# Kernel tuning notes

Hardware: AMD Instinct MI355X
Metric: run time of the kernel (lower is better)

Reference implementation:

```python
import jax, jax.numpy as jnp
import numpy as np

OBS_DIM = 768; H = 128; W = 128
OBJ_DIM = 128; REL_DIM = 64; N_SLOTS = 32; ACT_DIM = 16; HID = 256
EPS = 1e-8; DT = 0.1; N_ITERS = 3
REND_IN = OBJ_DIM * N_SLOTS + REL_DIM * N_SLOTS * N_SLOTS  # 69632


def _ln(x, g, b):
    m = x.mean(-1, keepdims=True)
    v = ((x - m) ** 2).mean(-1, keepdims=True)
    return (x - m) / jnp.sqrt(v + 1e-5) * g + b


def setup_inputs() -> dict:
    key = jax.random.key(0)
    ks = iter(jax.random.split(key, 48))

    def w(shape):
        fan = shape[-2] if len(shape) > 1 else shape[0]
        return jax.random.normal(next(ks), shape, jnp.float32) / np.sqrt(fan)

    d = {}
    d['obs'] = jax.random.normal(next(ks), (1, H, W, OBS_DIM), jnp.float32)
    d['action'] = jax.random.normal(next(ks), (1, ACT_DIM), jnp.float32)
    d['slot_noise'] = jax.random.normal(next(ks), (1, N_SLOTS, OBJ_DIM), jnp.float32)
    d['slots_mu'] = jax.random.normal(next(ks), (1, 1, OBJ_DIM), jnp.float32)
    d['slots_log_sigma'] = jax.random.normal(next(ks), (1, 1, OBJ_DIM), jnp.float32) * 0.1 - 1.0
    d['ln_in_g'] = jnp.ones((OBS_DIM,)); d['ln_in_b'] = jnp.zeros((OBS_DIM,))
    d['ln_s_g'] = jnp.ones((OBJ_DIM,)); d['ln_s_b'] = jnp.zeros((OBJ_DIM,))
    d['ln_m_g'] = jnp.ones((OBJ_DIM,)); d['ln_m_b'] = jnp.zeros((OBJ_DIM,))
    d['Wq'] = w((OBJ_DIM, OBJ_DIM)); d['Wk'] = w((OBS_DIM, OBJ_DIM)); d['Wv'] = w((OBS_DIM, OBJ_DIM))
    d['mlp_w1'] = w((OBJ_DIM, 2 * OBJ_DIM)); d['mlp_b1'] = jnp.zeros((2 * OBJ_DIM,))
    d['mlp_w2'] = w((2 * OBJ_DIM, OBJ_DIM)); d['mlp_b2'] = jnp.zeros((OBJ_DIM,))
    d['prop_w1'] = w((OBJ_DIM, HID)); d['prop_b1'] = jnp.zeros((HID,))
    d['prop_w2'] = w((HID, OBJ_DIM)); d['prop_b2'] = jnp.zeros((OBJ_DIM,))
    d['rel_w1'] = w((2 * OBJ_DIM, 2 * REL_DIM)); d['rel_b1'] = jnp.zeros((2 * REL_DIM,))
    d['rel_w2'] = w((2 * REL_DIM, REL_DIM)); d['rel_b2'] = jnp.zeros((REL_DIM,))
    d['dyn_w1'] = w((OBJ_DIM + ACT_DIM, HID)); d['dyn_b1'] = jnp.zeros((HID,))
    d['dyn_w2'] = w((HID, HID)); d['dyn_b2'] = jnp.zeros((HID,))
    d['dyn_w3'] = w((HID, OBJ_DIM)); d['dyn_b3'] = jnp.zeros((OBJ_DIM,))
    d['gravity'] = jnp.array([0.0, -9.8, 0.0], jnp.float32)
    d['rend_w1'] = w((REND_IN, 2 * OBS_DIM)); d['rend_b1'] = jnp.zeros((2 * OBS_DIM,))
    d['rend_w2'] = w((2 * OBS_DIM, OBS_DIM)); d['rend_b2'] = jnp.zeros((OBS_DIM,))
    return d


def reference(obs, action, slot_noise, slots_mu, slots_log_sigma,
              ln_in_g, ln_in_b, ln_s_g, ln_s_b, ln_m_g, ln_m_b,
              Wq, Wk, Wv, mlp_w1, mlp_b1, mlp_w2, mlp_b2,
              prop_w1, prop_b1, prop_w2, prop_b2,
              rel_w1, rel_b1, rel_w2, rel_b2,
              dyn_w1, dyn_b1, dyn_w2, dyn_b2, dyn_w3, dyn_b3,
              gravity, rend_w1, rend_b1, rend_w2, rend_b2):
    B = obs.shape[0]
    # --- slot attention over flattened feature map ---
    x = obs.reshape(B, -1, OBS_DIM)                 # [B, HW, C]
    x = _ln(x, ln_in_g, ln_in_b)
    k = x @ Wk                                      # [B, HW, D]
    v = x @ Wv                                      # [B, HW, D]
    slots = slots_mu + jnp.exp(slots_log_sigma) * slot_noise  # [B, S, D]
    scale = OBJ_DIM ** -0.5
    for _ in range(N_ITERS):
        prev = slots
        q = _ln(slots, ln_s_g, ln_s_b) @ Wq
        logits = jnp.einsum('bsd,bnd->bsn', q, k) * scale
        attn = jax.nn.softmax(logits, axis=1)       # softmax over slots (dim=1)
        attn = attn / (attn.sum(-1, keepdims=True) + EPS)
        slots = prev + jnp.einsum('bsn,bnd->bsd', attn, v)
        h = _ln(slots, ln_m_g, ln_m_b)
        slots = slots + (jax.nn.relu(h @ mlp_w1 + mlp_b1) @ mlp_w2 + mlp_b2)
    # --- object property decoding ---
    objects = jax.nn.relu(slots @ prop_w1 + prop_b1) @ prop_w2 + prop_b2  # [B, S, D]
    # --- pairwise relation encoding (O(S^2)) ---
    S = N_SLOTS
    oi = jnp.broadcast_to(objects[:, :, None, :], (B, S, S, OBJ_DIM))
    oj = jnp.broadcast_to(objects[:, None, :, :], (B, S, S, OBJ_DIM))
    pairs = jnp.concatenate([oi, oj], -1)            # [B, S, S, 2D]
    relations = jax.nn.relu(pairs @ rel_w1 + rel_b1) @ rel_w2 + rel_b2  # [B, S, S, REL]
    # --- scene graph takes batch element 0 (as in torch source) ---
    obj0 = objects[0:1]                              # [1, S, D]
    rel0 = relations[0]                              # [S, S, REL]
    # --- physics engine ---
    a = jnp.broadcast_to(action[:, None, :], (1, S, ACT_DIM))
    inp = jnp.concatenate([obj0, a], -1)
    h = jax.nn.relu(inp @ dyn_w1 + dyn_b1)
    h = jax.nn.relu(h @ dyn_w2 + dyn_b2)
    delta = h @ dyn_w3 + dyn_b3                      # [1, S, D]
    delta = delta.at[:, :, :3].add(gravity * DT)
    next_objects = obj0 + delta * DT                 # [1, S, D]
    # --- render next observation ---
    feat = jnp.concatenate([next_objects.reshape(1, -1), rel0.reshape(1, -1)], -1)
    next_obs = jax.nn.relu(feat @ rend_w1 + rend_b1) @ rend_w2 + rend_b2  # [1, OBS_DIM]
    return next_obs
```

## Files before the change

kernel.cpp:

```cpp
#include <hip/hip_runtime.h>
#include <hip/hip_bf16.h>
#include <math.h>

#define NPIX    16384
#define OBSD    768
#define OBJ     128
#define NS      32
#define HIDD    256
#define RELD    64
#define ACTD    16
#define QSCALE  0.08838834764831845f
#define LNEPS   1e-5f
#define ATEPS   1e-8f
#define DTC     0.1f

#define OFF_STATS 0
#define OFF_KV    (OFF_STATS + NPIX*2)
#define OFF_SLOTS (OFF_KV + NPIX*256)
#define OFF_Q     (OFF_SLOTS + 4096)
#define OFF_H     (OFF_Q + 4096)
#define OFF_APART (OFF_H + 4096)
#define OFF_OBJ   (OFF_APART + 256*4128)
#define OFF_FEAT  (OFF_OBJ + 4096)
#define OFF_P1    (OFF_FEAT + 69632)
#define OFF_HREND (OFF_P1 + 1024*1536)
#define OFF_P3    (OFF_HREND + 1536)

__global__ __launch_bounds__(256) void k_stats(const float* __restrict__ obs,
                                               float* __restrict__ stats)
{
    int lane = threadIdx.x & 63;
    int w    = threadIdx.x >> 6;
    int row  = blockIdx.x * 4 + w;
    const float* o = obs + (size_t)row * OBSD;
    float s = 0.f, s2 = 0.f;
    #pragma unroll
    for (int i = 0; i < 12; ++i) { float v = o[lane + 64*i]; s += v; s2 += v*v; }
    #pragma unroll
    for (int off = 32; off > 0; off >>= 1) {
        s  += __shfl_down(s,  off);
        s2 += __shfl_down(s2, off);
    }
    if (lane == 0) {
        float m   = s  * (1.f/OBSD);
        float var = s2 * (1.f/OBSD) - m*m;
        stats[row*2]   = m;
        stats[row*2+1] = rsqrtf(var + LNEPS);
    }
}

#define STA 129
__global__ __launch_bounds__(256) void k_kv(
    const float* __restrict__ obs, const float* __restrict__ stats,
    const float* __restrict__ g, const float* __restrict__ b,
    const float* __restrict__ Wk, const float* __restrict__ Wv,
    float* __restrict__ kv)
{
    __shared__ float As[32*STA];
    __shared__ float Bs[32*128];
    __shared__ float sm[128], sr[128];
    int t  = threadIdx.x;
    int m0 = blockIdx.x * 128;
    int nsel = blockIdx.y;
    const float* W = nsel ? Wv : Wk;
    int tx = t & 15, ty = t >> 4;
    float acc[8][8];
    #pragma unroll
    for (int i = 0; i < 8; ++i) {
        #pragma unroll
        for (int j = 0; j < 8; ++j) acc[i][j] = 0.f;
    }
    if (t < 128) { sm[t] = stats[(m0+t)*2]; sr[t] = stats[(m0+t)*2+1]; }

    for (int ks = 0; ks < 24; ++ks) {
        int k0 = ks * 32;
        __syncthreads();
        #pragma unroll
        for (int r = 0; r < 16; ++r) {
            int id = t + 256*r;
            int m  = id >> 5, kk = id & 31;
            float val = obs[(size_t)(m0+m)*OBSD + k0 + kk];
            val = (val - sm[m]) * sr[m] * g[k0+kk] + b[k0+kk];
            As[kk*STA + m] = val;
        }
        #pragma unroll
        for (int r = 0; r < 16; ++r) {
            int id = t + 256*r;
            int kk = id >> 7, jj = id & 127;
            Bs[kk*128 + jj] = W[(size_t)(k0+kk)*128 + jj];
        }
        __syncthreads();
        #pragma unroll
        for (int kk = 0; kk < 32; ++kk) {
            float a8[8], b8[8];
            #pragma unroll
            for (int i = 0; i < 8; ++i) a8[i] = As[kk*STA + ty*8 + i];
            float4 u0 = *(const float4*)&Bs[kk*128 + tx*8];
            float4 u1 = *(const float4*)&Bs[kk*128 + tx*8 + 4];
            b8[0]=u0.x; b8[1]=u0.y; b8[2]=u0.z; b8[3]=u0.w;
            b8[4]=u1.x; b8[5]=u1.y; b8[6]=u1.z; b8[7]=u1.w;
            #pragma unroll
            for (int i = 0; i < 8; ++i) {
                #pragma unroll
                for (int j = 0; j < 8; ++j)
                    acc[i][j] = fmaf(a8[i], b8[j], acc[i][j]);
            }
        }
    }
    #pragma unroll
    for (int i = 0; i < 8; ++i) {
        size_t row = (size_t)(m0 + ty*8 + i);
        float4 o0 = make_float4(acc[i][0], acc[i][1], acc[i][2], acc[i][3]);
        float4 o1 = make_float4(acc[i][4], acc[i][5], acc[i][6], acc[i][7]);
        *(float4*)&kv[row*256 + nsel*128 + tx*8]     = o0;
        *(float4*)&kv[row*256 + nsel*128 + tx*8 + 4] = o1;
    }
}

__global__ __launch_bounds__(256) void k_slots_init(
    const float* __restrict__ mu, const float* __restrict__ lsig,
    const float* __restrict__ noise, float* __restrict__ slots)
{
    int id = blockIdx.x * 256 + threadIdx.x;
    int d  = id & 127;
    slots[id] = mu[d] + expf(lsig[d]) * noise[id];
}

__global__ __launch_bounds__(128) void k_q(
    const float* __restrict__ slots, const float* __restrict__ Wq,
    const float* __restrict__ g, const float* __restrict__ b,
    float* __restrict__ qg)
{
    int s = blockIdx.x, t = threadIdx.x;
    float x = slots[s*128 + t];
    __shared__ float red[128];
    __shared__ float hh[128];
    red[t] = x; __syncthreads();
    for (int off = 64; off > 0; off >>= 1) { if (t < off) red[t] += red[t+off]; __syncthreads(); }
    float mean = red[0] * (1.f/128.f); __syncthreads();
    float dx = x - mean;
    red[t] = dx*dx; __syncthreads();
    for (int off = 64; off > 0; off >>= 1) { if (t < off) red[t] += red[t+off]; __syncthreads(); }
    float var = red[0] * (1.f/128.f);
    hh[t] = dx * rsqrtf(var + LNEPS) * g[t] + b[t];
    __syncthreads();
    float acc = 0.f;
    for (int d = 0; d < 128; ++d) acc = fmaf(hh[d], Wq[d*128 + t], acc);
    qg[s*128 + t] = acc;
}

#define STK 129
#define STQ 132
#define STT 36
__global__ __launch_bounds__(256) void k_attn(
    const float* __restrict__ kv, const float* __restrict__ qg,
    float* __restrict__ part)
{
    __shared__ float q_lds[NS*STQ];
    __shared__ float k_lds[64*STK];
    __shared__ float at[64*STT];
    int t   = threadIdx.x;
    int px0 = blockIdx.x * 64;
    #pragma unroll
    for (int r = 0; r < 16; ++r) {
        int id = t + 256*r;
        int s = id >> 7, d = id & 127;
        q_lds[s*STQ + d] = qg[id];
    }
    #pragma unroll
    for (int r = 0; r < 32; ++r) {
        int id = t + 256*r;
        int p = id >> 7, d = id & 127;
        k_lds[p*STK + d] = kv[(size_t)(px0+p)*256 + d];
    }
    __syncthreads();

    int wv = t >> 6, p = t & 63;
    float acc[8];
    #pragma unroll
    for (int u = 0; u < 8; ++u) acc[u] = 0.f;
    for (int dc = 0; dc < 4; ++dc) {
        float kr[32];
        #pragma unroll
        for (int d = 0; d < 32; ++d) kr[d] = k_lds[p*STK + dc*32 + d];
        #pragma unroll
        for (int u = 0; u < 8; ++u) {
            int s = u*4 + wv;
            const float* qp = &q_lds[s*STQ + dc*32];
            #pragma unroll
            for (int ii = 0; ii < 8; ++ii) {
                float4 q4 = *(const float4*)(qp + 4*ii);
                acc[u] = fmaf(q4.x, kr[4*ii+0], acc[u]);
                acc[u] = fmaf(q4.y, kr[4*ii+1], acc[u]);
                acc[u] = fmaf(q4.z, kr[4*ii+2], acc[u]);
                acc[u] = fmaf(q4.w, kr[4*ii+3], acc[u]);
            }
        }
    }
    #pragma unroll
    for (int u = 0; u < 8; ++u) at[p*STT + u*4 + wv] = acc[u] * QSCALE;
    __syncthreads();

    if (t < 64) {
        float mx = -1e30f;
        #pragma unroll
        for (int s = 0; s < NS; ++s) mx = fmaxf(mx, at[t*STT + s]);
        float smv = 0.f;
        #pragma unroll
        for (int s = 0; s < NS; ++s) { float e = expf(at[t*STT + s] - mx); at[t*STT + s] = e; smv += e; }
        float inv = 1.f / smv;
        #pragma unroll
        for (int s = 0; s < NS; ++s) at[t*STT + s] *= inv;
    }
    __syncthreads();

    int d = t & 127, sh = t >> 7;
    float u16[16];
    #pragma unroll
    for (int i = 0; i < 16; ++i) u16[i] = 0.f;
    const float* vbase = kv + (size_t)px0*256 + 128 + d;
    #pragma unroll 4
    for (int pp = 0; pp < 64; ++pp) {
        float vv = vbase[(size_t)pp*256];
        const float4* ap = (const float4*)&at[pp*STT + sh*16];
        #pragma unroll
        for (int gg = 0; gg < 4; ++gg) {
            float4 a4 = ap[gg];
            u16[4*gg+0] = fmaf(a4.x, vv, u16[4*gg+0]);
            u16[4*gg+1] = fmaf(a4.y, vv, u16[4*gg+1]);
            u16[4*gg+2] = fmaf(a4.z, vv, u16[4*gg+2]);
            u16[4*gg+3] = fmaf(a4.w, vv, u16[4*gg+3]);
        }
    }
    float* P = part + (size_t)blockIdx.x * 4128;
    #pragma unroll
    for (int g2 = 0; g2 < 16; ++g2) P[(sh*16 + g2)*128 + d] = u16[g2];
    if (t < 32) {
        float ss = 0.f;
        for (int pp = 0; pp < 64; ++pp) ss += at[pp*STT + t];
        P[4096 + t] = ss;
    }
}

__global__ __launch_bounds__(128) void k_update(
    const float* __restrict__ part, float* __restrict__ slots,
    float* __restrict__ hm, const float* __restrict__ g, const float* __restrict__ b)
{
    int s = blockIdx.x, t = threadIdx.x;
    float u = 0.f, ss = 0.f;
    for (int bb = 0; bb < 256; ++bb) {
        const float* P = part + (size_t)bb * 4128;
        u  += P[s*128 + t];
        ss += P[4096 + s];
    }
    float x = slots[s*128 + t] + u / (ss + ATEPS);
    __shared__ float red[128];
    red[t] = x; __syncthreads();
    for (int off = 64; off > 0; off >>= 1) { if (t < off) red[t] += red[t+off]; __syncthreads(); }
    float mean = red[0] * (1.f/128.f); __syncthreads();
    float dx = x - mean;
    red[t] = dx*dx; __syncthreads();
    for (int off = 64; off > 0; off >>= 1) { if (t < off) red[t] += red[t+off]; __syncthreads(); }
    float var = red[0] * (1.f/128.f);
    slots[s*128 + t] = x;
    hm[s*128 + t] = dx * rsqrtf(var + LNEPS) * g[t] + b[t];
}

__global__ __launch_bounds__(256) void k_mlp(
    const float* __restrict__ hm, const float* __restrict__ w1, const float* __restrict__ b1,
    const float* __restrict__ w2, const float* __restrict__ b2, float* __restrict__ slots)
{
    int s = blockIdx.x, t = threadIdx.x;
    __shared__ float h[128], hid[256];
    if (t < 128) h[t] = hm[s*128 + t];
    __syncthreads();
    float a = b1[t];
    for (int d = 0; d < 128; ++d) a = fmaf(h[d], w1[d*256 + t], a);
    hid[t] = fmaxf(a, 0.f);
    __syncthreads();
    if (t < 128) {
        float o = b2[t];
        for (int j = 0; j < 256; ++j) o = fmaf(hid[j], w2[j*128 + t], o);
        slots[s*128 + t] += o;
    }
}

__global__ __launch_bounds__(256) void k_prop(
    const float* __restrict__ slots, const float* __restrict__ w1, const float* __restrict__ b1,
    const float* __restrict__ w2, const float* __restrict__ b2, float* __restrict__ objects)
{
    int s = blockIdx.x, t = threadIdx.x;
    __shared__ float h[128], hid[256];
    if (t < 128) h[t] = slots[s*128 + t];
    __syncthreads();
    float a = b1[t];
    for (int d = 0; d < 128; ++d) a = fmaf(h[d], w1[d*256 + t], a);
    hid[t] = fmaxf(a, 0.f);
    __syncthreads();
    if (t < 128) {
        float o = b2[t];
        for (int j = 0; j < 256; ++j) o = fmaf(hid[j], w2[j*128 + t], o);
        objects[s*128 + t] = o;
    }
}

__global__ __launch_bounds__(128) void k_rel(
    const float* __restrict__ objects, const float* __restrict__ w1, const float* __restrict__ b1,
    const float* __restrict__ w2, const float* __restrict__ b2, float* __restrict__ rel_out)
{
    int pr = blockIdx.x; int i = pr >> 5, j = pr & 31; int t = threadIdx.x;
    __shared__ float pair[256], hid[128];
    pair[t]       = objects[i*128 + t];
    pair[128 + t] = objects[j*128 + t];
    __syncthreads();
    float a = b1[t];
    for (int c = 0; c < 256; ++c) a = fmaf(pair[c], w1[c*128 + t], a);
    hid[t] = fmaxf(a, 0.f);
    __syncthreads();
    if (t < 64) {
        float o = b2[t];
        for (int c = 0; c < 128; ++c) o = fmaf(hid[c], w2[c*64 + t], o);
        rel_out[(size_t)pr*64 + t] = o;
    }
}

__global__ __launch_bounds__(256) void k_dyn(
    const float* __restrict__ objects, const float* __restrict__ action,
    const float* __restrict__ w1, const float* __restrict__ b1,
    const float* __restrict__ w2, const float* __restrict__ b2,
    const float* __restrict__ w3, const float* __restrict__ b3,
    const float* __restrict__ gravity, float* __restrict__ feat)
{
    int s = blockIdx.x, t = threadIdx.x;
    __shared__ float inp[144], h1[256], h2[256];
    if (t < 128) inp[t] = objects[s*128 + t];
    else if (t < 144) inp[t] = action[t - 128];
    __syncthreads();
    float a = b1[t];
    for (int c = 0; c < 144; ++c) a = fmaf(inp[c], w1[c*256 + t], a);
    h1[t] = fmaxf(a, 0.f);
    __syncthreads();
    float a2 = b2[t];
    for (int c = 0; c < 256; ++c) a2 = fmaf(h1[c], w2[c*256 + t], a2);
    h2[t] = fmaxf(a2, 0.f);
    __syncthreads();
    if (t < 128) {
        float dlt = b3[t];
        for (int c = 0; c < 256; ++c) dlt = fmaf(h2[c], w3[c*128 + t], dlt);
        if (t < 3) dlt += gravity[t] * DTC;
        feat[s*128 + t] = objects[s*128 + t] + dlt * DTC;
    }
}

__global__ __launch_bounds__(384) void k_rend1(
    const float* __restrict__ feat, const float* __restrict__ w1, float* __restrict__ p1)
{
    int b = blockIdx.x, t = threadIdx.x;
    float4 acc = make_float4(0.f, 0.f, 0.f, 0.f);
    int i0 = b * 68;
    #pragma unroll 4
    for (int r = 0; r < 68; ++r) {
        int i = i0 + r;
        float f = feat[i];
        float4 w = *(const float4*)(w1 + (size_t)i * 1536 + 4*t);
        acc.x = fmaf(f, w.x, acc.x);
        acc.y = fmaf(f, w.y, acc.y);
        acc.z = fmaf(f, w.z, acc.z);
        acc.w = fmaf(f, w.w, acc.w);
    }
    *(float4*)(p1 + (size_t)b * 1536 + 4*t) = acc;
}

__global__ __launch_bounds__(256) void k_rend2(
    const float* __restrict__ p1, const float* __restrict__ b1, float* __restrict__ h)
{
    int j = blockIdx.x * 256 + threadIdx.x;
    float a0 = 0.f, a1 = 0.f, a2 = 0.f, a3 = 0.f;
    #pragma unroll 4
    for (int bb = 0; bb < 1024; bb += 4) {
        a0 += p1[(size_t)(bb+0)*1536 + j];
        a1 += p1[(size_t)(bb+1)*1536 + j];
        a2 += p1[(size_t)(bb+2)*1536 + j];
        a3 += p1[(size_t)(bb+3)*1536 + j];
    }
    h[j] = fmaxf((a0+a1) + (a2+a3) + b1[j], 0.f);
}

__global__ __launch_bounds__(256) void k_rend3(
    const float* __restrict__ h, const float* __restrict__ w2, float* __restrict__ p3)
{
    int bj = blockIdx.x, t = threadIdx.x;
    int j0 = bj * 32;
    float a0 = 0.f, a1 = 0.f, a2 = 0.f;
    #pragma unroll
    for (int j = 0; j < 32; ++j) {
        float hj = h[j0 + j];
        const float* w = w2 + (size_t)(j0 + j) * 768;
        a0 = fmaf(hj, w[t],       a0);
        a1 = fmaf(hj, w[t + 256], a1);
        a2 = fmaf(hj, w[t + 512], a2);
    }
    p3[(size_t)bj*768 + t]       = a0;
    p3[(size_t)bj*768 + t + 256] = a1;
    p3[(size_t)bj*768 + t + 512] = a2;
}

__global__ __launch_bounds__(256) void k_rend4(
    const float* __restrict__ p3, const float* __restrict__ b2, float* __restrict__ out)
{
    int m = blockIdx.x * 256 + threadIdx.x;
    float a = b2[m];
    #pragma unroll
    for (int bj = 0; bj < 48; ++bj) a += p3[(size_t)bj*768 + m];
    out[m] = a;
}

extern "C" void kernel_launch(void* const* d_in, const int* in_sizes, int n_in,
                              void* d_out, int out_size, void* d_ws, size_t ws_size,
                              hipStream_t stream) {
    (void)in_sizes; (void)n_in; (void)out_size; (void)ws_size;
    const float* obs      = (const float*)d_in[0];
    const float* action   = (const float*)d_in[1];
    const float* noise    = (const float*)d_in[2];
    const float* mu       = (const float*)d_in[3];
    const float* lsig     = (const float*)d_in[4];
    const float* ln_in_g  = (const float*)d_in[5];
    const float* ln_in_b  = (const float*)d_in[6];
    const float* ln_s_g   = (const float*)d_in[7];
    const float* ln_s_b   = (const float*)d_in[8];
    const float* ln_m_g   = (const float*)d_in[9];
    const float* ln_m_b   = (const float*)d_in[10];
    const float* Wq       = (const float*)d_in[11];
    const float* Wk       = (const float*)d_in[12];
    const float* Wv       = (const float*)d_in[13];
    const float* mlp_w1   = (const float*)d_in[14];
    const float* mlp_b1   = (const float*)d_in[15];
    const float* mlp_w2   = (const float*)d_in[16];
    const float* mlp_b2   = (const float*)d_in[17];
    const float* prop_w1  = (const float*)d_in[18];
    const float* prop_b1  = (const float*)d_in[19];
    const float* prop_w2  = (const float*)d_in[20];
    const float* prop_b2  = (const float*)d_in[21];
    const float* rel_w1   = (const float*)d_in[22];
    const float* rel_b1   = (const float*)d_in[23];
    const float* rel_w2   = (const float*)d_in[24];
    const float* rel_b2   = (const float*)d_in[25];
    const float* dyn_w1   = (const float*)d_in[26];
    const float* dyn_b1   = (const float*)d_in[27];
    const float* dyn_w2   = (const float*)d_in[28];
    const float* dyn_b2   = (const float*)d_in[29];
    const float* dyn_w3   = (const float*)d_in[30];
    const float* dyn_b3   = (const float*)d_in[31];
    const float* gravity  = (const float*)d_in[32];
    const float* rend_w1  = (const float*)d_in[33];
    const float* rend_b1  = (const float*)d_in[34];
    const float* rend_w2  = (const float*)d_in[35];
    const float* rend_b2  = (const float*)d_in[36];
    float* out = (float*)d_out;

    float* w      = (float*)d_ws;
    float* stats  = w + OFF_STATS;
    float* kv     = w + OFF_KV;
    float* slots  = w + OFF_SLOTS;
    float* qg     = w + OFF_Q;
    float* hm     = w + OFF_H;
    float* apart  = w + OFF_APART;
    float* objs   = w + OFF_OBJ;
    float* feat   = w + OFF_FEAT;
    float* relout = feat + 4096;
    float* p1     = w + OFF_P1;
    float* hrend  = w + OFF_HREND;
    float* p3     = w + OFF_P3;

    k_stats<<<4096, 256, 0, stream>>>(obs, stats);
    k_kv<<<dim3(128, 2), 256, 0, stream>>>(obs, stats, ln_in_g, ln_in_b, Wk, Wv, kv);
    k_slots_init<<<16, 256, 0, stream>>>(mu, lsig, noise, slots);

    for (int it = 0; it < 3; ++it) {
        k_q<<<32, 128, 0, stream>>>(slots, Wq, ln_s_g, ln_s_b, qg);
        k_attn<<<256, 256, 0, stream>>>(kv, qg, apart);
        k_update<<<32, 128, 0, stream>>>(apart, slots, hm, ln_m_g, ln_m_b);
        k_mlp<<<32, 256, 0, stream>>>(hm, mlp_w1, mlp_b1, mlp_w2, mlp_b2, slots);
    }

    k_prop<<<32, 256, 0, stream>>>(slots, prop_w1, prop_b1, prop_w2, prop_b2, objs);
    k_rel<<<1024, 128, 0, stream>>>(objs, rel_w1, rel_b1, rel_w2, rel_b2, relout);
    k_dyn<<<32, 256, 0, stream>>>(objs, action, dyn_w1, dyn_b1, dyn_w2, dyn_b2,
                                  dyn_w3, dyn_b3, gravity, feat);

    k_rend1<<<1024, 384, 0, stream>>>(feat, rend_w1, p1);
    k_rend2<<<6, 256, 0, stream>>>(p1, rend_b1, hrend);
    k_rend3<<<48, 256, 0, stream>>>(hrend, rend_w2, p3);
    k_rend4<<<3, 256, 0, stream>>>(p3, rend_b2, out);
}
```

Baseline: 1.105 ms.

## Double-buffer KV GEMM, fuse slot update/MLP/query and prop/dyn, split render reduction

The K/V projection GEMM now double-buffers its shared tiles with register prefetch and vectorized A reads, so global loads overlap compute and one barrier per k-step is dropped. The slot update, LayerNorm, MLP and next-iteration query projection are fused into one kernel, and the prop and dynamics MLPs are merged, which cuts several small launches. The render reduction over 1024 partials, previously done by only 6 blocks, is split into a two-stage reduction to expose more parallelism. Risks include higher register use in k_kv (launch bounds 256,1) and the extra syncs in the fused kernels.

```diff
diff --git a/kernel.cpp b/kernel.cpp
--- a/kernel.cpp
+++ b/kernel.cpp
@@ -25,6 +25,7 @@
 #define OFF_P1    (OFF_FEAT + 69632)
 #define OFF_HREND (OFF_P1 + 1024*1536)
 #define OFF_P3    (OFF_HREND + 1536)
+#define OFF_P2    (OFF_P3 + 48*768)
 
 __global__ __launch_bounds__(256) void k_stats(const float* __restrict__ obs,
                                                float* __restrict__ stats)
@@ -49,56 +50,71 @@
     }
 }
 
-#define STA 129
-__global__ __launch_bounds__(256) void k_kv(
+#define KVA 132
+__global__ __launch_bounds__(256, 1) void k_kv(
     const float* __restrict__ obs, const float* __restrict__ stats,
     const float* __restrict__ g, const float* __restrict__ b,
     const float* __restrict__ Wk, const float* __restrict__ Wv,
     float* __restrict__ kv)
 {
-    __shared__ float As[32*STA];
-    __shared__ float Bs[32*128];
-    __shared__ float sm[128], sr[128];
-    int t  = threadIdx.x;
-    int m0 = blockIdx.x * 128;
+    __shared__ float As[2][32*KVA];
+    __shared__ float Bs[2][32*128];
+    int t    = threadIdx.x;
+    int m0   = blockIdx.x * 128;
     int nsel = blockIdx.y;
     const float* W = nsel ? Wv : Wk;
     int tx = t & 15, ty = t >> 4;
+    int ka = t & 31, ma = t >> 5;
+    int jb = t & 127, kb = t >> 7;
+
     float acc[8][8];
     #pragma unroll
     for (int i = 0; i < 8; ++i) {
         #pragma unroll
         for (int j = 0; j < 8; ++j) acc[i][j] = 0.f;
     }
-    if (t < 128) { sm[t] = stats[(m0+t)*2]; sr[t] = stats[(m0+t)*2+1]; }
+
+    float smr[16], srr[16];
+    #pragma unroll
+    for (int r = 0; r < 16; ++r) {
+        smr[r] = stats[(size_t)(m0 + ma + 8*r)*2];
+        srr[r] = stats[(size_t)(m0 + ma + 8*r)*2 + 1];
+    }
+
+    float pa[16], pb[16], gv, cv;
+    #pragma unroll
+    for (int r = 0; r < 16; ++r) pa[r] = obs[(size_t)(m0 + ma + 8*r)*OBSD + ka];
+    #pragma unroll
+    for (int r = 0; r < 16; ++r) pb[r] = W[(size_t)(kb + 2*r)*128 + jb];
+    gv = g[ka]; cv = b[ka];
+    #pragma unroll
+    for (int r = 0; r < 16; ++r)
+        As[0][ka*KVA + ma + 8*r] = (pa[r] - smr[r]) * srr[r] * gv + cv;
+    #pragma unroll
+    for (int r = 0; r < 16; ++r)
+        Bs[0][(kb + 2*r)*128 + jb] = pb[r];
+    __syncthreads();
 
     for (int ks = 0; ks < 24; ++ks) {
-        int k0 = ks * 32;
-        __syncthreads();
-        #pragma unroll
-        for (int r = 0; r < 16; ++r) {
-            int id = t + 256*r;
-            int m  = id >> 5, kk = id & 31;
-            float val = obs[(size_t)(m0+m)*OBSD + k0 + kk];
-            val = (val - sm[m]) * sr[m] * g[k0+kk] + b[k0+kk];
-            As[kk*STA + m] = val;
+        int cur = ks & 1;
+        if (ks < 23) {
+            int k0 = (ks + 1) * 32;
+            #pragma unroll
+            for (int r = 0; r < 16; ++r)
+                pa[r] = obs[(size_t)(m0 + ma + 8*r)*OBSD + k0 + ka];
+            #pragma unroll
+            for (int r = 0; r < 16; ++r)
+                pb[r] = W[(size_t)(k0 + kb + 2*r)*128 + jb];
+            gv = g[k0 + ka]; cv = b[k0 + ka];
         }
         #pragma unroll
-        for (int r = 0; r < 16; ++r) {
-            int id = t + 256*r;
-            int kk = id >> 7, jj = id & 127;
-            Bs[kk*128 + jj] = W[(size_t)(k0+kk)*128 + jj];
-        }
-        __syncthreads();
-        #pragma unroll
         for (int kk = 0; kk < 32; ++kk) {
-            float a8[8], b8[8];
-            #pragma unroll
-            for (int i = 0; i < 8; ++i) a8[i] = As[kk*STA + ty*8 + i];
-            float4 u0 = *(const float4*)&Bs[kk*128 + tx*8];
-            float4 u1 = *(const float4*)&Bs[kk*128 + tx*8 + 4];
-            b8[0]=u0.x; b8[1]=u0.y; b8[2]=u0.z; b8[3]=u0.w;
-            b8[4]=u1.x; b8[5]=u1.y; b8[6]=u1.z; b8[7]=u1.w;
+            float4 a0 = *(const float4*)&As[cur][kk*KVA + ty*8];
+            float4 a1 = *(const float4*)&As[cur][kk*KVA + ty*8 + 4];
+            float4 u0 = *(const float4*)&Bs[cur][kk*128 + tx*8];
+            float4 u1 = *(const float4*)&Bs[cur][kk*128 + tx*8 + 4];
+            float a8[8] = {a0.x,a0.y,a0.z,a0.w,a1.x,a1.y,a1.z,a1.w};
+            float b8[8] = {u0.x,u0.y,u0.z,u0.w,u1.x,u1.y,u1.z,u1.w};
             #pragma unroll
             for (int i = 0; i < 8; ++i) {
                 #pragma unroll
@@ -106,7 +122,18 @@
                     acc[i][j] = fmaf(a8[i], b8[j], acc[i][j]);
             }
         }
-    }
+        if (ks < 23) {
+            int nb = cur ^ 1;
+            #pragma unroll
+            for (int r = 0; r < 16; ++r)
+                As[nb][ka*KVA + ma + 8*r] = (pa[r] - smr[r]) * srr[r] * gv + cv;
+            #pragma unroll
+            for (int r = 0; r < 16; ++r)
+                Bs[nb][(kb + 2*r)*128 + jb] = pb[r];
+        }
+        __syncthreads();
+    }
+
     #pragma unroll
     for (int i = 0; i < 8; ++i) {
         size_t row = (size_t)(m0 + ty*8 + i);
@@ -242,65 +269,126 @@
     }
 }
 
-__global__ __launch_bounds__(128) void k_update(
+__global__ __launch_bounds__(256) void k_umq(
     const float* __restrict__ part, float* __restrict__ slots,
-    float* __restrict__ hm, const float* __restrict__ g, const float* __restrict__ b)
+    const float* __restrict__ gm, const float* __restrict__ bm,
+    const float* __restrict__ w1, const float* __restrict__ b1,
+    const float* __restrict__ w2, const float* __restrict__ b2,
+    const float* __restrict__ gs, const float* __restrict__ bs,
+    const float* __restrict__ Wq, float* __restrict__ qg, int do_q)
 {
     int s = blockIdx.x, t = threadIdx.x;
+    int d = t & 127, half = t >> 7;
+    __shared__ float red[256];
+    __shared__ float ssred[2];
+    __shared__ float xs[128], hm[128], hid[256];
+
     float u = 0.f, ss = 0.f;
-    for (int bb = 0; bb < 256; ++bb) {
-        const float* P = part + (size_t)bb * 4128;
-        u  += P[s*128 + t];
+    const float* P0 = part + (size_t)(half * 128) * 4128;
+    for (int bb = 0; bb < 128; ++bb) {
+        const float* P = P0 + (size_t)bb * 4128;
+        u  += P[s*128 + d];
         ss += P[4096 + s];
     }
-    float x = slots[s*128 + t] + u / (ss + ATEPS);
-    __shared__ float red[128];
-    red[t] = x; __syncthreads();
-    for (int off = 64; off > 0; off >>= 1) { if (t < off) red[t] += red[t+off]; __syncthreads(); }
-    float mean = red[0] * (1.f/128.f); __syncthreads();
-    float dx = x - mean;
-    red[t] = dx*dx; __syncthreads();
-    for (int off = 64; off > 0; off >>= 1) { if (t < off) red[t] += red[t+off]; __syncthreads(); }
-    float var = red[0] * (1.f/128.f);
-    slots[s*128 + t] = x;
-    hm[s*128 + t] = dx * rsqrtf(var + LNEPS) * g[t] + b[t];
-}
-
-__global__ __launch_bounds__(256) void k_mlp(
-    const float* __restrict__ hm, const float* __restrict__ w1, const float* __restrict__ b1,
-    const float* __restrict__ w2, const float* __restrict__ b2, float* __restrict__ slots)
+    red[t] = u;
+    if (d == 0) ssred[half] = ss;
+    __syncthreads();
+    if (half == 0)
+        xs[d] = slots[s*128 + d] + (red[d] + red[d+128]) / (ssred[0] + ssred[1] + ATEPS);
+    __syncthreads();
+
+    red[t] = (half == 0) ? xs[d] : 0.f;
+    __syncthreads();
+    #pragma unroll
+    for (int off = 128; off > 0; off >>= 1) { if (t < off) red[t] += red[t+off]; __syncthreads(); }
+    float mean = red[0] * (1.f/128.f);
+    __syncthreads();
+    { float dx = (half == 0) ? (xs[d] - mean) : 0.f; red[t] = dx*dx; }
+    __syncthreads();
+    #pragma unroll
+    for (int off = 128; off > 0; off >>= 1) { if (t < off) red[t] += red[t+off]; __syncthreads(); }
+    float rstd = rsqrtf(red[0] * (1.f/128.f) + LNEPS);
+    __syncthreads();
+    if (half == 0) hm[d] = (xs[d] - mean) * rstd * gm[d] + bm[d];
+    __syncthreads();
+
+    float a = b1[t];
+    for (int c = 0; c < 128; ++c) a = fmaf(hm[c], w1[c*256 + t], a);
+    hid[t] = fmaxf(a, 0.f);
+    __syncthreads();
+    if (half == 0) {
+        float o = b2[d];
+        for (int j = 0; j < 256; ++j) o = fmaf(hid[j], w2[j*128 + d], o);
+        float xn = xs[d] + o;
+        slots[s*128 + d] = xn;
+        xs[d] = xn;
+    }
+    __syncthreads();
+
+    if (do_q) {
+        red[t] = (half == 0) ? xs[d] : 0.f;
+        __syncthreads();
+        #pragma unroll
+        for (int off = 128; off > 0; off >>= 1) { if (t < off) red[t] += red[t+off]; __syncthreads(); }
+        float m2 = red[0] * (1.f/128.f);
+        __syncthreads();
+        { float dx = (half == 0) ? (xs[d] - m2) : 0.f; red[t] = dx*dx; }
+        __syncthreads();
+        #pragma unroll
+        for (int off = 128; off > 0; off >>= 1) { if (t < off) red[t] += red[t+off]; __syncthreads(); }
+        float r2 = rsqrtf(red[0] * (1.f/128.f) + LNEPS);
+        __syncthreads();
+        if (half == 0) hm[d] = (xs[d] - m2) * r2 * gs[d] + bs[d];
+        __syncthreads();
+        float acc = 0.f;
+        for (int c = half*64; c < half*64 + 64; ++c) acc = fmaf(hm[c], Wq[c*128 + d], acc);
+        red[t] = acc;
+        __syncthreads();
+        if (half == 0) qg[s*128 + d] = red[d] + red[d+128];
+    }
+}
+
+__global__ __launch_bounds__(256) void k_propdyn(
+    const float* __restrict__ slots,
+    const float* __restrict__ pw1, const float* __restrict__ pb1,
+    const float* __restrict__ pw2, const float* __restrict__ pb2,
+    const float* __restrict__ action,
+    const float* __restrict__ dw1, const float* __restrict__ db1,
+    const float* __restrict__ dw2, const float* __restrict__ db2,
+    const float* __restrict__ dw3, const float* __restrict__ db3,
+    const float* __restrict__ gravity,
+    float* __restrict__ objects, float* __restrict__ feat)
 {
     int s = blockIdx.x, t = threadIdx.x;
-    __shared__ float h[128], hid[256];
-    if (t < 128) h[t] = hm[s*128 + t];
-    __syncthreads();
-    float a = b1[t];
-    for (int d = 0; d < 128; ++d) a = fmaf(h[d], w1[d*256 + t], a);
+    __shared__ float h[128], hid[256], inp[144], h2[256];
+    if (t < 128) h[t] = slots[s*128 + t];
+    __syncthreads();
+    float a = pb1[t];
+    for (int c = 0; c < 128; ++c) a = fmaf(h[c], pw1[c*256 + t], a);
     hid[t] = fmaxf(a, 0.f);
     __syncthreads();
     if (t < 128) {
-        float o = b2[t];
-        for (int j = 0; j < 256; ++j) o = fmaf(hid[j], w2[j*128 + t], o);
-        slots[s*128 + t] += o;
-    }
-}
-
-__global__ __launch_bounds__(256) void k_prop(
-    const float* __restrict__ slots, const float* __restrict__ w1, const float* __restrict__ b1,
-    const float* __restrict__ w2, const float* __restrict__ b2, float* __restrict__ objects)
-{
-    int s = blockIdx.x, t = threadIdx.x;
-    __shared__ float h[128], hid[256];
-    if (t < 128) h[t] = slots[s*128 + t];
-    __syncthreads();
-    float a = b1[t];
-    for (int d = 0; d < 128; ++d) a = fmaf(h[d], w1[d*256 + t], a);
-    hid[t] = fmaxf(a, 0.f);
+        float o = pb2[t];
+        for (int j = 0; j < 256; ++j) o = fmaf(hid[j], pw2[j*128 + t], o);
+        objects[s*128 + t] = o;
+        inp[t] = o;
+    } else if (t < 144) {
+        inp[t] = action[t - 128];
+    }
+    __syncthreads();
+    float a1 = db1[t];
+    for (int c = 0; c < 144; ++c) a1 = fmaf(inp[c], dw1[c*256 + t], a1);
+    hid[t] = fmaxf(a1, 0.f);
+    __syncthreads();
+    float a2 = db2[t];
+    for (int c = 0; c < 256; ++c) a2 = fmaf(hid[c], dw2[c*256 + t], a2);
+    h2[t] = fmaxf(a2, 0.f);
     __syncthreads();
     if (t < 128) {
-        float o = b2[t];
-        for (int j = 0; j < 256; ++j) o = fmaf(hid[j], w2[j*128 + t], o);
-        objects[s*128 + t] = o;
+        float dlt = db3[t];
+        for (int c = 0; c < 256; ++c) dlt = fmaf(h2[c], dw3[c*128 + t], dlt);
+        if (t < 3) dlt += gravity[t] * DTC;
+        feat[s*128 + t] = inp[t] + dlt * DTC;
     }
 }
 
@@ -321,34 +409,6 @@
         float o = b2[t];
         for (int c = 0; c < 128; ++c) o = fmaf(hid[c], w2[c*64 + t], o);
         rel_out[(size_t)pr*64 + t] = o;
-    }
-}
-
-__global__ __launch_bounds__(256) void k_dyn(
-    const float* __restrict__ objects, const float* __restrict__ action,
-    const float* __restrict__ w1, const float* __restrict__ b1,
-    const float* __restrict__ w2, const float* __restrict__ b2,
-    const float* __restrict__ w3, const float* __restrict__ b3,
-    const float* __restrict__ gravity, float* __restrict__ feat)
-{
-    int s = blockIdx.x, t = threadIdx.x;
-    __shared__ float inp[144], h1[256], h2[256];
-    if (t < 128) inp[t] = objects[s*128 + t];
-    else if (t < 144) inp[t] = action[t - 128];
-    __syncthreads();
-    float a = b1[t];
-    for (int c = 0; c < 144; ++c) a = fmaf(inp[c], w1[c*256 + t], a);
-    h1[t] = fmaxf(a, 0.f);
-    __syncthreads();
-    float a2 = b2[t];
-    for (int c = 0; c < 256; ++c) a2 = fmaf(h1[c], w2[c*256 + t], a2);
-    h2[t] = fmaxf(a2, 0.f);
-    __syncthreads();
-    if (t < 128) {
-        float dlt = b3[t];
-        for (int c = 0; c < 256; ++c) dlt = fmaf(h2[c], w3[c*128 + t], dlt);
-        if (t < 3) dlt += gravity[t] * DTC;
-        feat[s*128 + t] = objects[s*128 + t] + dlt * DTC;
     }
 }
 
@@ -371,19 +431,31 @@
     *(float4*)(p1 + (size_t)b * 1536 + 4*t) = acc;
 }
 
-__global__ __launch_bounds__(256) void k_rend2(
-    const float* __restrict__ p1, const float* __restrict__ b1, float* __restrict__ h)
-{
-    int j = blockIdx.x * 256 + threadIdx.x;
+__global__ __launch_bounds__(256) void k_rend2a(
+    const float* __restrict__ p1, float* __restrict__ p2)
+{
+    int j  = blockIdx.x * 256 + threadIdx.x;
+    int sl = blockIdx.y;
+    const float* P = p1 + (size_t)sl * 64 * 1536;
     float a0 = 0.f, a1 = 0.f, a2 = 0.f, a3 = 0.f;
     #pragma unroll 4
-    for (int bb = 0; bb < 1024; bb += 4) {
-        a0 += p1[(size_t)(bb+0)*1536 + j];
-        a1 += p1[(size_t)(bb+1)*1536 + j];
-        a2 += p1[(size_t)(bb+2)*1536 + j];
-        a3 += p1[(size_t)(bb+3)*1536 + j];
-    }
-    h[j] = fmaxf((a0+a1) + (a2+a3) + b1[j], 0.f);
+    for (int bb = 0; bb < 64; bb += 4) {
+        a0 += P[(size_t)(bb+0)*1536 + j];
+        a1 += P[(size_t)(bb+1)*1536 + j];
+        a2 += P[(size_t)(bb+2)*1536 + j];
+        a3 += P[(size_t)(bb+3)*1536 + j];
+    }
+    p2[sl*1536 + j] = (a0+a1) + (a2+a3);
+}
+
+__global__ __launch_bounds__(256) void k_rend2b(
+    const float* __restrict__ p2, const float* __restrict__ b1, float* __restrict__ h)
+{
+    int j = blockIdx.x * 256 + threadIdx.x;
+    float a = b1[j];
+    #pragma unroll
+    for (int sl = 0; sl < 16; ++sl) a += p2[sl*1536 + j];
+    h[j] = fmaxf(a, 0.f);
 }
 
 __global__ __launch_bounds__(256) void k_rend3(
@@ -463,7 +535,6 @@
     float* kv     = w + OFF_KV;
     float* slots  = w + OFF_SLOTS;
     float* qg     = w + OFF_Q;
-    float* hm     = w + OFF_H;
     float* apart  = w + OFF_APART;
     float* objs   = w + OFF_OBJ;
     float* feat   = w + OFF_FEAT;
@@ -471,25 +542,28 @@
     float* p1     = w + OFF_P1;
     float* hrend  = w + OFF_HREND;
     float* p3     = w + OFF_P3;
+    float* p2     = w + OFF_P2;
 
     k_stats<<<4096, 256, 0, stream>>>(obs, stats);
     k_kv<<<dim3(128, 2), 256, 0, stream>>>(obs, stats, ln_in_g, ln_in_b, Wk, Wv, kv);
     k_slots_init<<<16, 256, 0, stream>>>(mu, lsig, noise, slots);
+    k_q<<<32, 128, 0, stream>>>(slots, Wq, ln_s_g, ln_s_b, qg);
 
     for (int it = 0; it < 3; ++it) {
-        k_q<<<32, 128, 0, stream>>>(slots, Wq, ln_s_g, ln_s_b, qg);
         k_attn<<<256, 256, 0, stream>>>(kv, qg, apart);
-        k_update<<<32, 128, 0, stream>>>(apart, slots, hm, ln_m_g, ln_m_b);
-        k_mlp<<<32, 256, 0, stream>>>(hm, mlp_w1, mlp_b1, mlp_w2, mlp_b2, slots);
-    }
-
-    k_prop<<<32, 256, 0, stream>>>(slots, prop_w1, prop_b1, prop_w2, prop_b2, objs);
+        k_umq<<<32, 256, 0, stream>>>(apart, slots, ln_m_g, ln_m_b,
+                                      mlp_w1, mlp_b1, mlp_w2, mlp_b2,
+                                      ln_s_g, ln_s_b, Wq, qg, (it < 2) ? 1 : 0);
+    }
+
+    k_propdyn<<<32, 256, 0, stream>>>(slots, prop_w1, prop_b1, prop_w2, prop_b2,
+                                      action, dyn_w1, dyn_b1, dyn_w2, dyn_b2,
+                                      dyn_w3, dyn_b3, gravity, objs, feat);
     k_rel<<<1024, 128, 0, stream>>>(objs, rel_w1, rel_b1, rel_w2, rel_b2, relout);
-    k_dyn<<<32, 256, 0, stream>>>(objs, action, dyn_w1, dyn_b1, dyn_w2, dyn_b2,
-                                  dyn_w3, dyn_b3, gravity, feat);
 
     k_rend1<<<1024, 384, 0, stream>>>(feat, rend_w1, p1);
-    k_rend2<<<6, 256, 0, stream>>>(p1, rend_b1, hrend);
+    k_rend2a<<<dim3(6, 16), 256, 0, stream>>>(p1, p2);
+    k_rend2b<<<6, 256, 0, stream>>>(p2, rend_b1, hrend);
     k_rend3<<<48, 256, 0, stream>>>(hrend, rend_w2, p3);
     k_rend4<<<3, 256, 0, stream>>>(p3, rend_b2, out);
 }
```

New measurement: 2.359 ms. 2.14x slower.
